# Performance work log

Hardware: AMD Instinct MI355X
Metric: run time of the kernel (lower is better)

## Reference

```python
import jax, jax.numpy as jnp
import numpy as np

N = 100000      # num_nodes
E = 400000      # num edges
HID = 128       # hidden_channels (== in_channels, memory dim)
OUT = 64        # out_channels (per head)
HEADS = 4
HD = HEADS * OUT  # 256, TransformerConv concat output dim


def _lin(k, fan_in, fan_out):
    return jax.random.normal(k, (fan_in, fan_out), jnp.float32) * 0.02


def setup_inputs() -> dict:
    key = jax.random.key(0)
    ks = jax.random.split(key, 16)
    return {
        "edge_index": jax.random.randint(ks[0], (2, E), 0, N, dtype=jnp.int64),
        "edge_time": jax.random.randint(ks[1], (E, 1), 0, 1000000, dtype=jnp.int64),
        "x": jax.random.normal(ks[2], (N, HID), jnp.float32),
        "memory": jax.random.normal(ks[3], (N, HID), jnp.float32),  # TGN memory table (detached in fwd)
        # TransformerConv params (lin_query / lin_key / lin_value / lin_skip, all with bias)
        "Wq": _lin(ks[4], HID, HD), "bq": jnp.zeros((HD,), jnp.float32),
        "Wk": _lin(ks[5], HID, HD), "bk": jnp.zeros((HD,), jnp.float32),
        "Wv": _lin(ks[6], HID, HD), "bv": jnp.zeros((HD,), jnp.float32),
        "Wskip": _lin(ks[7], HID, HD), "bskip": jnp.zeros((HD,), jnp.float32),
        # rating MLP: Linear(512,128) -> ReLU -> Linear(128,64) -> ReLU -> Linear(64,1)
        "W1": _lin(ks[8], 2 * HD, 128), "b1": jnp.zeros((128,), jnp.float32),
        "W2": _lin(ks[9], 128, 64), "b2": jnp.zeros((64,), jnp.float32),
        "W3": _lin(ks[10], 64, 1), "b3": jnp.zeros((1,), jnp.float32),
    }


def reference(edge_index, edge_time, x, memory,
              Wq, bq, Wk, bk, Wv, bv, Wskip, bskip,
              W1, b1, W2, b2, W3, b3):
    src, dst = edge_index[0], edge_index[1]
    n = x.shape[0]

    # x = memory.detach() + x
    h = memory + x  # [N, HID]

    # TransformerConv (heads=4, concat=True, root_weight=True)
    q = (h @ Wq + bq).reshape(n, HEADS, OUT)
    k = (h @ Wk + bk).reshape(n, HEADS, OUT)
    v = (h @ Wv + bv).reshape(n, HEADS, OUT)

    # per-edge attention scores: messages flow src -> dst, softmax over in-edges of dst
    scores = jnp.sum(q[dst] * k[src], axis=-1) / jnp.sqrt(jnp.float32(OUT))  # [E, H]
    smax = jax.ops.segment_max(scores, dst, num_segments=n)                   # [N, H]
    e = jnp.exp(scores - smax[dst])
    denom = jax.ops.segment_sum(e, dst, num_segments=n)
    alpha = e / (denom[dst] + 1e-16)                                          # [E, H]

    agg = jax.ops.segment_sum(alpha[:, :, None] * v[src], dst, num_segments=n)  # [N, H, OUT]
    out = agg.reshape(n, HD) + (h @ Wskip + bskip)                              # skip connection

    # interaction embeddings + MLP head (dropout inactive at eval)
    inter = jnp.concatenate([out[src], out[dst]], axis=-1)  # [E, 512]
    hdd = jax.nn.relu(inter @ W1 + b1)
    hdd = jax.nn.relu(hdd @ W2 + b2)
    rating = jax.nn.sigmoid(hdd @ W3 + b3) * 4.0 + 1.0
    return rating[:, 0]
```

## Files before the change

### kernel.cpp

```cpp
#include <hip/hip_runtime.h>
#include <math.h>

#define N_NODES 100000
#define N_EDGES 400000
#define HID 128
#define HEADS 4
#define OUT_C 64
#define HD 256
#define SCAN_CHUNK 1024
#define NB_SCAN ((N_NODES + SCAN_CHUNK - 1) / SCAN_CHUNK)

typedef __attribute__((ext_vector_type(8))) short bf16x8;
typedef __attribute__((ext_vector_type(4))) float f32x4;

__device__ __forceinline__ unsigned short fbf(float f) {
    unsigned u = __float_as_uint(f);
    unsigned r = (u + 0x7fffu + ((u >> 16) & 1u)) >> 16;
    return (unsigned short)r;
}
__device__ __forceinline__ float bf2f(unsigned short u) {
    return __uint_as_float(((unsigned)u) << 16);
}

__global__ __launch_bounds__(256) void init_zero(int* __restrict__ deg,
                                                 int* __restrict__ cursor) {
    int i = blockIdx.x * 256 + threadIdx.x;
    if (i < N_NODES) { deg[i] = 0; cursor[i] = 0; }
}

__global__ __launch_bounds__(256) void k_deg(const int* __restrict__ ei,
                                             int* __restrict__ deg) {
    int e = blockIdx.x * 256 + threadIdx.x;
    if (e < N_EDGES) atomicAdd(&deg[ei[N_EDGES + e]], 1);
}

__global__ __launch_bounds__(256) void k_scan1(const int* __restrict__ deg,
                                               int* __restrict__ rp,
                                               int* __restrict__ bsum) {
    __shared__ int ts[256];
    int b = blockIdx.x, t = threadIdx.x;
    int base = b * SCAN_CHUNK + t * 4;
    int vv[4];
    int s = 0;
#pragma unroll
    for (int i = 0; i < 4; ++i) {
        int d = (base + i < N_NODES) ? deg[base + i] : 0;
        vv[i] = s;
        s += d;
    }
    ts[t] = s;
    __syncthreads();
    for (int off = 1; off < 256; off <<= 1) {
        int x = (t >= off) ? ts[t - off] : 0;
        __syncthreads();
        ts[t] += x;
        __syncthreads();
    }
    int ex = ts[t] - s;
#pragma unroll
    for (int i = 0; i < 4; ++i)
        if (base + i < N_NODES) rp[base + i] = ex + vv[i];
    if (t == 255) bsum[b] = ts[255];
}

__global__ __launch_bounds__(256) void k_scan2(int* __restrict__ bsum) {
    __shared__ int ts[256];
    int t = threadIdx.x;
    int v = (t < NB_SCAN) ? bsum[t] : 0;
    ts[t] = v;
    __syncthreads();
    for (int off = 1; off < 256; off <<= 1) {
        int x = (t >= off) ? ts[t - off] : 0;
        __syncthreads();
        ts[t] += x;
        __syncthreads();
    }
    if (t < NB_SCAN) bsum[t] = ts[t] - v;
}

__global__ __launch_bounds__(256) void k_scan3(int* __restrict__ rp,
                                               const int* __restrict__ bsum) {
    int i = blockIdx.x * 256 + threadIdx.x;
    if (i < N_NODES) rp[i] += bsum[i / SCAN_CHUNK];
}

__global__ __launch_bounds__(256) void k_bucket(const int* __restrict__ ei,
                                                const int* __restrict__ rp,
                                                int* __restrict__ cursor,
                                                int* __restrict__ csr_src,
                                                int* __restrict__ csr_dst,
                                                int* __restrict__ csr_eid) {
    int e = blockIdx.x * 256 + threadIdx.x;
    if (e >= N_EDGES) return;
    int src = ei[e];
    int d   = ei[N_EDGES + e];
    int idx = atomicAdd(&cursor[d], 1);
    int s   = rp[d] + idx;
    csr_src[s] = src;
    csr_dst[s] = d;
    csr_eid[s] = e;
}

__global__ __launch_bounds__(256) void pack_wg(
    const float* __restrict__ Wq, const float* __restrict__ Wk,
    const float* __restrict__ Wv, const float* __restrict__ Ws,
    unsigned short* __restrict__ Wp) {
    int i = blockIdx.x * 256 + threadIdx.x;
    if (i >= 16384) return;
    int lane = i & 63, nt = (i >> 6) & 15, kt = (i >> 10) & 3, z = i >> 12;
    const float* W = (z == 0) ? Wq : (z == 1) ? Wk : (z == 2) ? Wv : Ws;
    int q = lane >> 4, c = lane & 15;
#pragma unroll
    for (int j = 0; j < 8; ++j)
        Wp[i * 8 + j] = fbf(W[(kt * 32 + q * 8 + j) * HD + nt * 16 + c]);
}

__global__ __launch_bounds__(256) void pack_wc(const float* __restrict__ W1,
                                               unsigned short* __restrict__ Wcp) {
    int i = blockIdx.x * 256 + threadIdx.x;
    if (i >= 8192) return;
    int lane = i & 63, nt = (i >> 6) & 15, kt = i >> 10;
    int q = lane >> 4, c = lane & 15;
    int n = nt * 16 + c;
#pragma unroll
    for (int j = 0; j < 8; ++j) {
        int k = kt * 32 + q * 8 + j;
        float v = (n < 128) ? W1[k * 128 + n] : W1[(k + 256) * 128 + (n - 128)];
        Wcp[i * 8 + j] = fbf(v);
    }
}

__global__ __launch_bounds__(256) void pack_w2(const float* __restrict__ W2,
                                               unsigned short* __restrict__ W2p) {
    int i = blockIdx.x * 256 + threadIdx.x;
    if (i >= 1024) return;
    int lane = i & 63, nt = (i >> 6) & 3, kt = i >> 8;
    int q = lane >> 4, c = lane & 15;
#pragma unroll
    for (int j = 0; j < 8; ++j)
        W2p[i * 8 + j] = fbf(W2[(kt * 32 + q * 8 + j) * 64 + nt * 16 + c]);
}

__global__ __launch_bounds__(256) void gemm_proj(
    const float* __restrict__ x, const float* __restrict__ mem,
    const unsigned short* __restrict__ Wp,
    const float* __restrict__ bq, const float* __restrict__ bk,
    const float* __restrict__ bv, const float* __restrict__ bs,
    unsigned short* __restrict__ Q, unsigned short* __restrict__ K,
    unsigned short* __restrict__ V, unsigned short* __restrict__ S)
{
    __shared__ __align__(16) short As[64 * 136];
    __shared__ __align__(16) short Slab[4 * 64 * 68];

    const int t = threadIdx.x;
    const int w = t >> 6, l = t & 63;
    const int q = l >> 4, c = l & 15;
    const int m0 = blockIdx.x * 64;

    {
        const float4* x4 = (const float4*)x;
        const float4* m4 = (const float4*)mem;
#pragma unroll
        for (int j = 0; j < 8; ++j) {
            int idx = t + j * 256;
            int row = idx >> 5, c4 = idx & 31;
            int gr  = m0 + row;
            ushort4 hv = make_ushort4(0, 0, 0, 0);
            if (gr < N_NODES) {
                float4 a = x4[(size_t)gr * 32 + c4];
                float4 b = m4[(size_t)gr * 32 + c4];
                hv = make_ushort4(fbf(a.x + b.x), fbf(a.y + b.y),
                                  fbf(a.z + b.z), fbf(a.w + b.w));
            }
            *(ushort4*)&As[row * 136 + c4 * 4] = hv;
        }
    }
    __syncthreads();

    short* slab = &Slab[w * 64 * 68];
    const int srow = l >> 3;
    const int schk = l & 7;

    for (int z = 0; z < 4; ++z) {
        const float* bz = (z == 0) ? bq : (z == 1) ? bk : (z == 2) ? bv : bs;
        unsigned short* Oz = (z == 0) ? Q : (z == 1) ? K : (z == 2) ? V : S;

        f32x4 acc[4][4];
#pragma unroll
        for (int mt = 0; mt < 4; ++mt)
#pragma unroll
            for (int nt = 0; nt < 4; ++nt) acc[mt][nt] = (f32x4){0.f, 0.f, 0.f, 0.f};

#pragma unroll
        for (int kt = 0; kt < 4; ++kt) {
            bf16x8 af[4];
#pragma unroll
            for (int mt = 0; mt < 4; ++mt)
                af[mt] = *(const bf16x8*)&As[(mt * 16 + c) * 136 + kt * 32 + q * 8];
#pragma unroll
            for (int nt = 0; nt < 4; ++nt) {
                int ntg = w * 4 + nt;
                bf16x8 bv8 = *(const bf16x8*)&Wp[(size_t)(((z * 4 + kt) * 16 + ntg) * 64 + l) * 8];
#pragma unroll
                for (int mt = 0; mt < 4; ++mt)
                    acc[mt][nt] = __builtin_amdgcn_mfma_f32_16x16x32_bf16(af[mt], bv8, acc[mt][nt], 0, 0, 0);
            }
        }

#pragma unroll
        for (int nt = 0; nt < 4; ++nt) {
            float bb = bz[w * 64 + nt * 16 + c];
#pragma unroll
            for (int mt = 0; mt < 4; ++mt)
#pragma unroll
                for (int r = 0; r < 4; ++r)
                    slab[(mt * 16 + q * 4 + r) * 68 + nt * 16 + c] =
                        (short)fbf(acc[mt][nt][r] + bb);
        }
#pragma unroll
        for (int j = 0; j < 8; ++j) {
            int row = j * 8 + srow;
            int gr = m0 + row;
            if (gr < N_NODES)
                *(bf16x8*)&Oz[(size_t)gr * HD + w * 64 + schk * 8] =
                    *(const bf16x8*)&slab[row * 68 + schk * 8];
        }
    }
}

__global__ __launch_bounds__(256) void k_attn(
    const int* __restrict__ rp, const int* __restrict__ deg,
    const int* __restrict__ csr_src,
    const unsigned short* __restrict__ Q, const unsigned short* __restrict__ K,
    const unsigned short* __restrict__ V, const unsigned short* __restrict__ S,
    unsigned short* __restrict__ out)
{
    int node = blockIdx.x * 4 + (threadIdx.x >> 6);
    int l = threadIdx.x & 63;
    if (node >= N_NODES) return;
    int start = rp[node];
    int cnt   = deg[node];

    float q0, q1, q2, q3;
    {
        ushort4 u = *(const ushort4*)&Q[(size_t)node * HD + l * 4];
        q0 = bf2f(u.x); q1 = bf2f(u.y); q2 = bf2f(u.z); q3 = bf2f(u.w);
    }

    float m = -1e30f, d = 0.f;
    float a0 = 0.f, a1 = 0.f, a2 = 0.f, a3 = 0.f;

    for (int i = 0; i < cnt; ++i) {
        int src = csr_src[start + i];
        ushort4 ku = *(const ushort4*)&K[(size_t)src * HD + l * 4];
        float s = q0 * bf2f(ku.x) + q1 * bf2f(ku.y) + q2 * bf2f(ku.z) + q3 * bf2f(ku.w);
        s += __shfl_xor(s, 1);
        s += __shfl_xor(s, 2);
        s += __shfl_xor(s, 4);
        s += __shfl_xor(s, 8);
        s *= 0.125f;

        float mn    = fmaxf(m, s);
        float scale = __expf(m - mn);
        float e     = __expf(s - mn);
        d = d * scale + e;
        ushort4 vu = *(const ushort4*)&V[(size_t)src * HD + l * 4];
        a0 = a0 * scale + e * bf2f(vu.x);
        a1 = a1 * scale + e * bf2f(vu.y);
        a2 = a2 * scale + e * bf2f(vu.z);
        a3 = a3 * scale + e * bf2f(vu.w);
        m = mn;
    }

    float inv = 1.f / (d + 1e-16f);
    ushort4 su = *(const ushort4*)&S[(size_t)node * HD + l * 4];
    ushort4 ov = make_ushort4(fbf(bf2f(su.x) + a0 * inv),
                              fbf(bf2f(su.y) + a1 * inv),
                              fbf(bf2f(su.z) + a2 * inv),
                              fbf(bf2f(su.w) + a3 * inv));
    *(ushort4*)&out[(size_t)node * HD + l * 4] = ov;
}

__global__ __launch_bounds__(256) void pd_gemm(
    const unsigned short* __restrict__ outb,
    const unsigned short* __restrict__ Wcp,
    unsigned short* __restrict__ PD)
{
    __shared__ __align__(16) char sh[4 * 64 * 68 * 2];
    short* As   = (short*)sh;
    short* Slab = (short*)sh;

    const int t = threadIdx.x;
    const int w = t >> 6, l = t & 63;
    const int q = l >> 4, c = l & 15;
    const int m0 = blockIdx.x * 64;

#pragma unroll
    for (int j = 0; j < 8; ++j) {
        int idx = t + j * 256;
        int row = idx >> 5, c4 = idx & 31;
        int gr  = m0 + row;
        bf16x8 v = (bf16x8){0,0,0,0,0,0,0,0};
        if (gr < N_NODES)
            v = *(const bf16x8*)&outb[(size_t)gr * HD + c4 * 8];
        *(bf16x8*)&As[row * 264 + c4 * 8] = v;
    }
    __syncthreads();

    f32x4 acc[4][4];
#pragma unroll
    for (int mt = 0; mt < 4; ++mt)
#pragma unroll
        for (int nt = 0; nt < 4; ++nt) acc[mt][nt] = (f32x4){0.f, 0.f, 0.f, 0.f};

#pragma unroll
    for (int kt = 0; kt < 8; ++kt) {
        bf16x8 af[4];
#pragma unroll
        for (int mt = 0; mt < 4; ++mt)
            af[mt] = *(const bf16x8*)&As[(mt * 16 + c) * 264 + kt * 32 + q * 8];
#pragma unroll
        for (int nt = 0; nt < 4; ++nt) {
            int ntg = w * 4 + nt;
            bf16x8 bv8 = *(const bf16x8*)&Wcp[(size_t)((kt * 16 + ntg) * 64 + l) * 8];
#pragma unroll
            for (int mt = 0; mt < 4; ++mt)
                acc[mt][nt] = __builtin_amdgcn_mfma_f32_16x16x32_bf16(af[mt], bv8, acc[mt][nt], 0, 0, 0);
        }
    }
    __syncthreads();

    short* slab = &Slab[w * 64 * 68];
#pragma unroll
    for (int nt = 0; nt < 4; ++nt)
#pragma unroll
        for (int mt = 0; mt < 4; ++mt)
#pragma unroll
            for (int r = 0; r < 4; ++r)
                slab[(mt * 16 + q * 4 + r) * 68 + nt * 16 + c] =
                    (short)fbf(acc[mt][nt][r]);
    const int srow = l >> 3, schk = l & 7;
#pragma unroll
    for (int j = 0; j < 8; ++j) {
        int row = j * 8 + srow;
        int gr = m0 + row;
        if (gr < N_NODES)
            *(bf16x8*)&PD[(size_t)gr * HD + w * 64 + schk * 8] =
                *(const bf16x8*)&slab[row * 68 + schk * 8];
    }
}

__global__ __launch_bounds__(256) void edge_mlp_pd(
    const int* __restrict__ csr_src, const int* __restrict__ csr_dst,
    const int* __restrict__ csr_eid,
    const unsigned short* __restrict__ PD,
    const float* __restrict__ b1,
    const unsigned short* __restrict__ W2p, const float* __restrict__ b2,
    const float* __restrict__ W3, const float* __restrict__ b3,
    float* __restrict__ rating)
{
    __shared__ __align__(16) char lds[64 * 136 * 2];
    short* h1t = (short*)lds;
    float* h2s = (float*)lds;

    const int t = threadIdx.x;
    const int w = t >> 6, l = t & 63;
    const int q = l >> 4, c = l & 15;
    const int e0 = blockIdx.x * 64;

#pragma unroll
    for (int j = 0; j < 4; ++j) {
        int idx = t + j * 256;
        int row = idx >> 4, ch = idx & 15;
        int src = csr_src[e0 + row];
        int dst = csr_dst[e0 + row];
        bf16x8 pv = *(const bf16x8*)&PD[(size_t)src * HD + ch * 8];
        bf16x8 dv = *(const bf16x8*)&PD[(size_t)dst * HD + 128 + ch * 8];
        float4 ba = *(const float4*)&b1[ch * 8];
        float4 bb = *(const float4*)&b1[ch * 8 + 4];
        bf16x8 hv;
        hv[0] = (short)fbf(fmaxf(bf2f((unsigned short)pv[0]) + bf2f((unsigned short)dv[0]) + ba.x, 0.f));
        hv[1] = (short)fbf(fmaxf(bf2f((unsigned short)pv[1]) + bf2f((unsigned short)dv[1]) + ba.y, 0.f));
        hv[2] = (short)fbf(fmaxf(bf2f((unsigned short)pv[2]) + bf2f((unsigned short)dv[2]) + ba.z, 0.f));
        hv[3] = (short)fbf(fmaxf(bf2f((unsigned short)pv[3]) + bf2f((unsigned short)dv[3]) + ba.w, 0.f));
        hv[4] = (short)fbf(fmaxf(bf2f((unsigned short)pv[4]) + bf2f((unsigned short)dv[4]) + bb.x, 0.f));
        hv[5] = (short)fbf(fmaxf(bf2f((unsigned short)pv[5]) + bf2f((unsigned short)dv[5]) + bb.y, 0.f));
        hv[6] = (short)fbf(fmaxf(bf2f((unsigned short)pv[6]) + bf2f((unsigned short)dv[6]) + bb.z, 0.f));
        hv[7] = (short)fbf(fmaxf(bf2f((unsigned short)pv[7]) + bf2f((unsigned short)dv[7]) + bb.w, 0.f));
        *(bf16x8*)&h1t[row * 136 + ch * 8] = hv;
    }
    __syncthreads();

    f32x4 acc2[4];
#pragma unroll
    for (int i = 0; i < 4; ++i) acc2[i] = (f32x4){0.f, 0.f, 0.f, 0.f};
#pragma unroll
    for (int kt = 0; kt < 4; ++kt) {
        bf16x8 av = *(const bf16x8*)&h1t[(w * 16 + c) * 136 + kt * 32 + q * 8];
#pragma unroll
        for (int nt = 0; nt < 4; ++nt) {
            bf16x8 bv = *(const bf16x8*)&W2p[(size_t)((kt * 4 + nt) * 64 + l) * 8];
            acc2[nt] = __builtin_amdgcn_mfma_f32_16x16x32_bf16(av, bv, acc2[nt], 0, 0, 0);
        }
    }
    __syncthreads();

#pragma unroll
    for (int nt = 0; nt < 4; ++nt) {
        float bv = b2[nt * 16 + c];
#pragma unroll
        for (int r = 0; r < 4; ++r)
            h2s[(w * 16 + q * 4 + r) * 65 + nt * 16 + c] = fmaxf(acc2[nt][r] + bv, 0.f);
    }
    __syncthreads();

    if (t < 64) {
        float a = b3[0];
#pragma unroll 8
        for (int kk = 0; kk < 64; ++kk)
            a += h2s[t * 65 + kk] * W3[kk];
        rating[csr_eid[e0 + t]] = 4.f / (1.f + __expf(-a)) + 1.f;
    }
}

extern "C" void kernel_launch(void* const* d_in, const int* in_sizes, int n_in,
                              void* d_out, int out_size, void* d_ws, size_t ws_size,
                              hipStream_t stream) {
    const int*   ei  = (const int*)d_in[0];
    const float* x   = (const float*)d_in[2];
    const float* mem = (const float*)d_in[3];
    const float* Wq  = (const float*)d_in[4];
    const float* bq  = (const float*)d_in[5];
    const float* Wk  = (const float*)d_in[6];
    const float* bk  = (const float*)d_in[7];
    const float* Wv  = (const float*)d_in[8];
    const float* bv  = (const float*)d_in[9];
    const float* Ws  = (const float*)d_in[10];
    const float* bs  = (const float*)d_in[11];
    const float* W1  = (const float*)d_in[12];
    const float* b1  = (const float*)d_in[13];
    const float* W2  = (const float*)d_in[14];
    const float* b2  = (const float*)d_in[15];
    const float* W3  = (const float*)d_in[16];
    const float* b3  = (const float*)d_in[17];
    float* rating = (float*)d_out;

    unsigned short* Q = (unsigned short*)d_ws;
    const size_t NHDe = (size_t)N_NODES * HD;
    unsigned short* K = Q + NHDe;
    unsigned short* V = K + NHDe;
    unsigned short* S = V + NHDe;
    int* rp      = (int*)(S + NHDe);
    int* deg     = rp + N_NODES;
    int* cursor  = deg + N_NODES;
    int* csr_src = cursor + N_NODES;
    int* csr_dst = csr_src + N_EDGES;
    int* csr_eid = csr_dst + N_EDGES;
    int* bsum    = csr_eid + N_EDGES;
    unsigned short* Wp  = (unsigned short*)(bsum + 128);
    unsigned short* Wcp = Wp + 16384 * 8;
    unsigned short* W2p = Wcp + 8192 * 8;
    unsigned short* PD  = K;

    const int nblk  = (N_NODES + 255) / 256;
    const int eblk  = (N_EDGES + 255) / 256;
    const int wgrid = (N_NODES + 3) / 4;

    init_zero<<<nblk, 256, 0, stream>>>(deg, cursor);
    k_deg<<<eblk, 256, 0, stream>>>(ei, deg);
    k_scan1<<<NB_SCAN, 256, 0, stream>>>(deg, rp, bsum);
    k_scan2<<<1, 256, 0, stream>>>(bsum);
    k_scan3<<<nblk, 256, 0, stream>>>(rp, bsum);
    k_bucket<<<eblk, 256, 0, stream>>>(ei, rp, cursor, csr_src, csr_dst, csr_eid);
    pack_wg<<<64, 256, 0, stream>>>(Wq, Wk, Wv, Ws, Wp);
    pack_wc<<<32, 256, 0, stream>>>(W1, Wcp);
    pack_w2<<<4, 256, 0, stream>>>(W2, W2p);

    gemm_proj<<<(N_NODES + 63) / 64, 256, 0, stream>>>(
        x, mem, Wp, bq, bk, bv, bs, Q, K, V, S);

    k_attn<<<wgrid, 256, 0, stream>>>(rp, deg, csr_src, Q, K, V, S, Q);

    pd_gemm<<<(N_NODES + 63) / 64, 256, 0, stream>>>(Q, Wcp, PD);

    edge_mlp_pd<<<N_EDGES / 64, 256, 0, stream>>>(
        csr_src, csr_dst, csr_eid, PD, b1, W2p, b2, W3, b3, rating);
}
```

Baseline: 499.7 us.

## Interleave K and V per node and store GEMM output directly from MFMA

K and V projections are written into one interleaved KV buffer, so each attention lane fetches its 4 K and 4 V values with a single 16-byte gather per source node instead of two separate 8-byte gathers. The projection and PD GEMMs swap MFMA operands so each lane holds four consecutive output columns, letting results go straight to global memory as ushort4 stores and dropping the LDS staging slab and a barrier. The trade-off is narrower, less coalesced 8-byte global stores in the GEMM epilogues and a changed workspace layout.

```diff
diff --git a/kernel.cpp b/kernel.cpp
--- a/kernel.cpp
+++ b/kernel.cpp
@@ -146,11 +146,10 @@
     const unsigned short* __restrict__ Wp,
     const float* __restrict__ bq, const float* __restrict__ bk,
     const float* __restrict__ bv, const float* __restrict__ bs,
-    unsigned short* __restrict__ Q, unsigned short* __restrict__ K,
-    unsigned short* __restrict__ V, unsigned short* __restrict__ S)
+    unsigned short* __restrict__ Q, unsigned short* __restrict__ KV,
+    unsigned short* __restrict__ S)
 {
     __shared__ __align__(16) short As[64 * 136];
-    __shared__ __align__(16) short Slab[4 * 64 * 68];
 
     const int t = threadIdx.x;
     const int w = t >> 6, l = t & 63;
@@ -177,13 +176,10 @@
     }
     __syncthreads();
 
-    short* slab = &Slab[w * 64 * 68];
-    const int srow = l >> 3;
-    const int schk = l & 7;
+    const int nbase = w * 64 + q * 4;
 
     for (int z = 0; z < 4; ++z) {
         const float* bz = (z == 0) ? bq : (z == 1) ? bk : (z == 2) ? bv : bs;
-        unsigned short* Oz = (z == 0) ? Q : (z == 1) ? K : (z == 2) ? V : S;
 
         f32x4 acc[4][4];
 #pragma unroll
@@ -193,37 +189,42 @@
 
 #pragma unroll
         for (int kt = 0; kt < 4; ++kt) {
-            bf16x8 af[4];
+            bf16x8 nf[4];
 #pragma unroll
             for (int mt = 0; mt < 4; ++mt)
-                af[mt] = *(const bf16x8*)&As[(mt * 16 + c) * 136 + kt * 32 + q * 8];
+                nf[mt] = *(const bf16x8*)&As[(mt * 16 + c) * 136 + kt * 32 + q * 8];
 #pragma unroll
             for (int nt = 0; nt < 4; ++nt) {
                 int ntg = w * 4 + nt;
-                bf16x8 bv8 = *(const bf16x8*)&Wp[(size_t)(((z * 4 + kt) * 16 + ntg) * 64 + l) * 8];
+                bf16x8 wf = *(const bf16x8*)&Wp[(size_t)(((z * 4 + kt) * 16 + ntg) * 64 + l) * 8];
 #pragma unroll
                 for (int mt = 0; mt < 4; ++mt)
-                    acc[mt][nt] = __builtin_amdgcn_mfma_f32_16x16x32_bf16(af[mt], bv8, acc[mt][nt], 0, 0, 0);
+                    acc[mt][nt] = __builtin_amdgcn_mfma_f32_16x16x32_bf16(wf, nf[mt], acc[mt][nt], 0, 0, 0);
             }
         }
 
 #pragma unroll
         for (int nt = 0; nt < 4; ++nt) {
-            float bb = bz[w * 64 + nt * 16 + c];
-#pragma unroll
-            for (int mt = 0; mt < 4; ++mt)
-#pragma unroll
-                for (int r = 0; r < 4; ++r)
-                    slab[(mt * 16 + q * 4 + r) * 68 + nt * 16 + c] =
-                        (short)fbf(acc[mt][nt][r] + bb);
-        }
-#pragma unroll
-        for (int j = 0; j < 8; ++j) {
-            int row = j * 8 + srow;
-            int gr = m0 + row;
-            if (gr < N_NODES)
-                *(bf16x8*)&Oz[(size_t)gr * HD + w * 64 + schk * 8] =
-                    *(const bf16x8*)&slab[row * 68 + schk * 8];
+            int nb = nbase + nt * 16;
+            float4 bb = *(const float4*)&bz[nb];
+#pragma unroll
+            for (int mt = 0; mt < 4; ++mt) {
+                int node = m0 + mt * 16 + c;
+                if (node < N_NODES) {
+                    ushort4 o = make_ushort4(fbf(acc[mt][nt][0] + bb.x),
+                                             fbf(acc[mt][nt][1] + bb.y),
+                                             fbf(acc[mt][nt][2] + bb.z),
+                                             fbf(acc[mt][nt][3] + bb.w));
+                    if (z == 0)
+                        *(ushort4*)&Q[(size_t)node * HD + nb] = o;
+                    else if (z == 1)
+                        *(ushort4*)&KV[(size_t)node * 512 + nb * 2] = o;
+                    else if (z == 2)
+                        *(ushort4*)&KV[(size_t)node * 512 + nb * 2 + 4] = o;
+                    else
+                        *(ushort4*)&S[(size_t)node * HD + nb] = o;
+                }
+            }
         }
     }
 }
@@ -231,8 +232,8 @@
 __global__ __launch_bounds__(256) void k_attn(
     const int* __restrict__ rp, const int* __restrict__ deg,
     const int* __restrict__ csr_src,
-    const unsigned short* __restrict__ Q, const unsigned short* __restrict__ K,
-    const unsigned short* __restrict__ V, const unsigned short* __restrict__ S,
+    const unsigned short* __restrict__ Q, const unsigned short* __restrict__ KV,
+    const unsigned short* __restrict__ S,
     unsigned short* __restrict__ out)
 {
     int node = blockIdx.x * 4 + (threadIdx.x >> 6);
@@ -252,8 +253,9 @@
 
     for (int i = 0; i < cnt; ++i) {
         int src = csr_src[start + i];
-        ushort4 ku = *(const ushort4*)&K[(size_t)src * HD + l * 4];
-        float s = q0 * bf2f(ku.x) + q1 * bf2f(ku.y) + q2 * bf2f(ku.z) + q3 * bf2f(ku.w);
+        bf16x8 kv = *(const bf16x8*)&KV[(size_t)src * 512 + l * 8];
+        float s = q0 * bf2f((unsigned short)kv[0]) + q1 * bf2f((unsigned short)kv[1])
+                + q2 * bf2f((unsigned short)kv[2]) + q3 * bf2f((unsigned short)kv[3]);
         s += __shfl_xor(s, 1);
         s += __shfl_xor(s, 2);
         s += __shfl_xor(s, 4);
@@ -264,11 +266,10 @@
         float scale = __expf(m - mn);
         float e     = __expf(s - mn);
         d = d * scale + e;
-        ushort4 vu = *(const ushort4*)&V[(size_t)src * HD + l * 4];
-        a0 = a0 * scale + e * bf2f(vu.x);
-        a1 = a1 * scale + e * bf2f(vu.y);
-        a2 = a2 * scale + e * bf2f(vu.z);
-        a3 = a3 * scale + e * bf2f(vu.w);
+        a0 = a0 * scale + e * bf2f((unsigned short)kv[4]);
+        a1 = a1 * scale + e * bf2f((unsigned short)kv[5]);
+        a2 = a2 * scale + e * bf2f((unsigned short)kv[6]);
+        a3 = a3 * scale + e * bf2f((unsigned short)kv[7]);
         m = mn;
     }
 
@@ -286,9 +287,7 @@
     const unsigned short* __restrict__ Wcp,
     unsigned short* __restrict__ PD)
 {
-    __shared__ __align__(16) char sh[4 * 64 * 68 * 2];
-    short* As   = (short*)sh;
-    short* Slab = (short*)sh;
+    __shared__ __align__(16) short As[64 * 264];
 
     const int t = threadIdx.x;
     const int w = t >> 6, l = t & 63;
@@ -315,38 +314,33 @@
 
 #pragma unroll
     for (int kt = 0; kt < 8; ++kt) {
-        bf16x8 af[4];
+        bf16x8 nf[4];
 #pragma unroll
         for (int mt = 0; mt < 4; ++mt)
-            af[mt] = *(const bf16x8*)&As[(mt * 16 + c) * 264 + kt * 32 + q * 8];
+            nf[mt] = *(const bf16x8*)&As[(mt * 16 + c) * 264 + kt * 32 + q * 8];
 #pragma unroll
         for (int nt = 0; nt < 4; ++nt) {
             int ntg = w * 4 + nt;
-            bf16x8 bv8 = *(const bf16x8*)&Wcp[(size_t)((kt * 16 + ntg) * 64 + l) * 8];
+            bf16x8 wf = *(const bf16x8*)&Wcp[(size_t)((kt * 16 + ntg) * 64 + l) * 8];
 #pragma unroll
             for (int mt = 0; mt < 4; ++mt)
-                acc[mt][nt] = __builtin_amdgcn_mfma_f32_16x16x32_bf16(af[mt], bv8, acc[mt][nt], 0, 0, 0);
-        }
-    }
-    __syncthreads();
-
-    short* slab = &Slab[w * 64 * 68];
-#pragma unroll
-    for (int nt = 0; nt < 4; ++nt)
-#pragma unroll
-        for (int mt = 0; mt < 4; ++mt)
-#pragma unroll
-            for (int r = 0; r < 4; ++r)
-                slab[(mt * 16 + q * 4 + r) * 68 + nt * 16 + c] =
-                    (short)fbf(acc[mt][nt][r]);
-    const int srow = l >> 3, schk = l & 7;
-#pragma unroll
-    for (int j = 0; j < 8; ++j) {
-        int row = j * 8 + srow;
-        int gr = m0 + row;
-        if (gr < N_NODES)
-            *(bf16x8*)&PD[(size_t)gr * HD + w * 64 + schk * 8] =
-                *(const bf16x8*)&slab[row * 68 + schk * 8];
+                acc[mt][nt] = __builtin_amdgcn_mfma_f32_16x16x32_bf16(wf, nf[mt], acc[mt][nt], 0, 0, 0);
+        }
+    }
+
+    const int nbase = w * 64 + q * 4;
+#pragma unroll
+    for (int nt = 0; nt < 4; ++nt) {
+        int nb = nbase + nt * 16;
+#pragma unroll
+        for (int mt = 0; mt < 4; ++mt) {
+            int node = m0 + mt * 16 + c;
+            if (node < N_NODES) {
+                ushort4 o = make_ushort4(fbf(acc[mt][nt][0]), fbf(acc[mt][nt][1]),
+                                         fbf(acc[mt][nt][2]), fbf(acc[mt][nt][3]));
+                *(ushort4*)&PD[(size_t)node * HD + nb] = o;
+            }
+        }
     }
 }
 
@@ -445,11 +439,10 @@
     const float* b3  = (const float*)d_in[17];
     float* rating = (float*)d_out;
 
-    unsigned short* Q = (unsigned short*)d_ws;
+    unsigned short* Q  = (unsigned short*)d_ws;
     const size_t NHDe = (size_t)N_NODES * HD;
-    unsigned short* K = Q + NHDe;
-    unsigned short* V = K + NHDe;
-    unsigned short* S = V + NHDe;
+    unsigned short* KV = Q + NHDe;
+    unsigned short* S  = KV + 2 * NHDe;
     int* rp      = (int*)(S + NHDe);
     int* deg     = rp + N_NODES;
     int* cursor  = deg + N_NODES;
@@ -460,7 +453,7 @@
     unsigned short* Wp  = (unsigned short*)(bsum + 128);
     unsigned short* Wcp = Wp + 16384 * 8;
     unsigned short* W2p = Wcp + 8192 * 8;
-    unsigned short* PD  = K;
+    unsigned short* PD  = KV;
 
     const int nblk  = (N_NODES + 255) / 256;
     const int eblk  = (N_EDGES + 255) / 256;
@@ -477,9 +470,9 @@
     pack_w2<<<4, 256, 0, stream>>>(W2, W2p);
 
     gemm_proj<<<(N_NODES + 63) / 64, 256, 0, stream>>>(
-        x, mem, Wp, bq, bk, bv, bs, Q, K, V, S);
-
-    k_attn<<<wgrid, 256, 0, stream>>>(rp, deg, csr_src, Q, K, V, S, Q);
+        x, mem, Wp, bq, bk, bv, bs, Q, KV, S);
+
+    k_attn<<<wgrid, 256, 0, stream>>>(rp, deg, csr_src, Q, KV, S, Q);
 
     pd_gemm<<<(N_NODES + 63) / 64, 256, 0, stream>>>(Q, Wcp, PD);
 
```

New measurement: 518.3 us. +3.7%, slower.
